# Optimization experiments

Hardware: AMD Instinct MI355X
Metric: run time of the kernel (lower is better)

The kernel has to match this reference:

```python
import jax, jax.numpy as jnp
import numpy as np
import math

D_MODEL = 1024
NUM_HEADS = 16
THETA = 10000.0


def _rope(x, pos):
    # x: [B, H, S, d_k]; pos: [S] int -- complex rotation on interleaved pairs
    d_k = x.shape[-1]
    inv_freq = 1.0 / (THETA ** (jnp.arange(0, d_k, 2, dtype=jnp.float32) / d_k))  # [d_k/2]
    angles = pos.astype(jnp.float32)[:, None] * inv_freq[None, :]  # [S, d_k/2]
    cos, sin = jnp.cos(angles), jnp.sin(angles)
    xe = x[..., 0::2]  # real parts
    xo = x[..., 1::2]  # imag parts
    out = jnp.stack([xe * cos - xo * sin, xe * sin + xo * cos], axis=-1)
    return out.reshape(x.shape)


def setup_inputs() -> dict:
    key = jax.random.key(0)
    k1, k2, k3 = jax.random.split(key, 3)
    B, S, D = 2, 2048, D_MODEL
    w_std = math.sqrt(2.0 / (D + 3 * D))
    o_std = math.sqrt(2.0 / (D + D))
    return {
        "x": jax.random.normal(k1, (B, S, D), dtype=jnp.float32),
        "token_positions": jnp.arange(S, dtype=jnp.int32),
        "w_qkv": jax.random.normal(k2, (3 * D, D), dtype=jnp.float32) * w_std,
        "w_out": jax.random.normal(k3, (D, D), dtype=jnp.float32) * o_std,
    }


def reference(x, token_positions, w_qkv, w_out):
    B, S, D = x.shape
    H = NUM_HEADS
    d_k = D // H

    qkv = jnp.einsum('bsd,ed->bse', x, w_qkv)  # [B, S, 3D]
    q, k, v = jnp.split(qkv, 3, axis=-1)

    def to_heads(t):
        return t.reshape(B, S, H, d_k).transpose(0, 2, 1, 3)  # [B, H, S, d_k]

    q, k, v = to_heads(q), to_heads(k), to_heads(v)
    q = _rope(q, token_positions)
    k = _rope(k, token_positions)

    scores = jnp.einsum('bhqd,bhkd->bhqk', q, k) / math.sqrt(d_k)
    causal = jnp.tril(jnp.ones((S, S), dtype=bool))
    scores = jnp.where(causal, scores, -jnp.inf)
    attn = jax.nn.softmax(scores, axis=-1)
    out = jnp.einsum('bhqk,bhkd->bhqd', attn, v)  # [B, H, S, d_k]
    out = out.transpose(0, 2, 1, 3).reshape(B, S, D)
    return jnp.einsum('bsd,ed->bse', out, w_out)
```

## Files before the change

### kernel.cpp

```cpp
#include <hip/hip_runtime.h>

typedef unsigned short u16;
typedef unsigned int u32;
typedef __attribute__((ext_vector_type(8))) __bf16 bf16x8;
typedef __attribute__((ext_vector_type(4))) float f32x4;
typedef __attribute__((ext_vector_type(4))) u32 u32x4;
typedef __attribute__((ext_vector_type(4))) u16 u16x4;

#define DEV __device__ __forceinline__

constexpr int S_LEN = 2048;
constexpr int DMODEL = 1024;
constexpr int NHEAD = 16;
constexpr int ROWS = 4096;
constexpr int LDP = 1056;
constexpr float QSCALE = 0.125f * 1.4426950408889634f;

DEV u16 f2bf(float f) {
  union { float f; u32 u; } v; v.f = f;
  u32 u = v.u;
  u32 r = (u + 0x7fffu + ((u >> 16) & 1u)) >> 16;
  return (u16)r;
}
DEV float vexp2(float x) {
#if __has_builtin(__builtin_amdgcn_exp2f)
  return __builtin_amdgcn_exp2f(x);
#else
  return exp2f(x);
#endif
}
DEV int swz(int r, int c) { return r * 64 + (c ^ ((r & 7) << 3)); }

__global__ __launch_bounds__(256) void k_cvt_all(const float* __restrict__ x,
                                                 const float* __restrict__ wq,
                                                 const float* __restrict__ wo,
                                                 u16* __restrict__ xb,
                                                 u16* __restrict__ wqb,
                                                 u16* __restrict__ wob) {
  int i = blockIdx.x * 256 + threadIdx.x;
  const float* in; u16* out; int off;
  if (i < 524288)       { in = x;  out = xb;  off = i; }
  else if (i < 917504)  { in = wq; out = wqb; off = i - 524288; }
  else                  { in = wo; out = wob; off = i - 917504; }
  const float4* p4 = (const float4*)in;
  float4 a = p4[2 * off], b = p4[2 * off + 1];
  alignas(16) u16 r[8] = {f2bf(a.x), f2bf(a.y), f2bf(a.z), f2bf(a.w),
                          f2bf(b.x), f2bf(b.y), f2bf(b.z), f2bf(b.w)};
  int row = off >> 7, oct = off & 127;
  *(u32x4*)(out + (size_t)row * LDP + oct * 8) = *(const u32x4*)r;
}

__global__ __launch_bounds__(256) void k_rope_tab(const int* __restrict__ pos,
                                                  float2* __restrict__ tab) {
  int t = blockIdx.x * 256 + threadIdx.x;
  int s = t >> 5, fi = t & 31;
  float p = (float)pos[s];
  float invf = expf(-(float)fi * 0.28782313662425572f);
  float ang = p * invf;
  tab[t] = float2{cosf(ang), sinf(ang)};
}

template <int BM, int MODE>
__global__ __launch_bounds__(256, 4) void k_gemm(const u16* __restrict__ A, int lda,
                                                 const u16* __restrict__ Bw, int ldb,
                                                 void* __restrict__ Out,
                                                 u16* __restrict__ vt,
                                                 const float2* __restrict__ tab,
                                                 int NB) {
  constexpr int MR = BM / 32;
  constexpr int NA = BM / 64;
  __shared__ alignas(16) u16 As[2][BM * 32];
  __shared__ alignas(16) u16 Bs[2][128 * 32];
  const int tid = threadIdx.x, lane = tid & 63;
  const int w = tid >> 6, wr = w >> 1, wc = w & 1;
  const int l15 = lane & 15, l16 = lane >> 4;
  const int cpx = gridDim.x >> 3;
  const int wg = (blockIdx.x & 7) * cpx + (blockIdx.x >> 3);
  const int mb = wg / NB, nb = wg - mb * NB;
  const int m0 = mb * BM, n0 = nb * 128;

  const int grow = tid >> 2, gc = tid & 3;
  const u16* aP = A + (size_t)(m0 + grow) * lda + gc * 8;
  const u16* bP = Bw + (size_t)(n0 + grow) * ldb + gc * 8;
  const size_t aStep = (size_t)64 * lda;
  const size_t bStep = (size_t)64 * ldb;
  const int wrI = grow * 32 + ((gc ^ (grow & 3)) << 3);

  u32x4 ra0, ra1, rb0, rb1;
#define LOADT(t) do { \
    ra0 = *(const u32x4*)(aP + (t) * 32); \
    if (NA == 2) ra1 = *(const u32x4*)(aP + aStep + (t) * 32); \
    rb0 = *(const u32x4*)(bP + (t) * 32); \
    rb1 = *(const u32x4*)(bP + bStep + (t) * 32); \
  } while (0)
#define WRITET(bufc) do { \
    *(u32x4*)&As[bufc][wrI] = ra0; \
    if (NA == 2) *(u32x4*)&As[bufc][wrI + 2048] = ra1; \
    *(u32x4*)&Bs[bufc][wrI] = rb0; \
    *(u32x4*)&Bs[bufc][wrI + 2048] = rb1; \
  } while (0)

  f32x4 acc[MR][4] = {};
  const int x3 = l15 & 3;

#define COMPUTE(bufc) do { \
    bf16x8 af[MR]; \
    _Pragma("unroll") \
    for (int m_ = 0; m_ < MR; m_++) \
      af[m_] = *(const bf16x8*)&As[bufc][(wr * (BM / 2) + m_ * 16 + l15) * 32 + \
                                         (((l16 ^ x3)) << 3)]; \
    __builtin_amdgcn_s_setprio(1); \
    _Pragma("unroll") \
    for (int n_ = 0; n_ < 4; n_++) { \
      bf16x8 bb = *(const bf16x8*)&Bs[bufc][(wc * 64 + n_ * 16 + l15) * 32 + \
                                            (((l16 ^ x3)) << 3)]; \
      _Pragma("unroll") \
      for (int m_ = 0; m_ < MR; m_++) \
        acc[m_][n_] = __builtin_amdgcn_mfma_f32_16x16x32_bf16(af[m_], bb, acc[m_][n_], 0, 0, 0); \
    } \
    __builtin_amdgcn_s_setprio(0); \
  } while (0)

#define BAR() do { \
    asm volatile("s_waitcnt lgkmcnt(0)" ::: "memory"); \
    __builtin_amdgcn_s_barrier(); \
  } while (0)

  LOADT(0);
  WRITET(0);
  LOADT(1);
  BAR();

  for (int t = 0; t < 32; ++t) {
    COMPUTE(t & 1);
    if (t + 1 < 32) WRITET((t + 1) & 1);
    if (t + 2 < 32) LOADT(t + 2);
    BAR();
  }
#undef LOADT
#undef WRITET
#undef COMPUTE
#undef BAR

  const int rb = m0 + wr * (BM / 2) + l16 * 4;
  const int cb = n0 + wc * 64 + l15;
  if (MODE == 0) {
    float* o = (float*)Out;
#pragma unroll
    for (int m = 0; m < MR; m++)
#pragma unroll
      for (int n = 0; n < 4; n++)
#pragma unroll
        for (int r = 0; r < 4; r++)
          o[(size_t)(rb + m * 16 + r) * 1024 + cb + n * 16] = acc[m][n][r];
  } else if (n0 >= 2048) {
#pragma unroll
    for (int m = 0; m < MR; m++)
#pragma unroll
      for (int n = 0; n < 4; n++) {
        int row = rb + m * 16, col = cb + n * 16;
        int bb = row >> 11, s = row & 2047, hd = col - 2048;
        u16x4 pk = {f2bf(acc[m][n][0]), f2bf(acc[m][n][1]),
                    f2bf(acc[m][n][2]), f2bf(acc[m][n][3])};
        *(u16x4*)&vt[(size_t)(bb * 1024 + hd) * S_LEN + s] = pk;
      }
  } else {
    u16* qk = (u16*)Out;
    const bool isq = (n0 < 1024);
#pragma unroll
    for (int m = 0; m < MR; m++) {
      int row0 = rb + m * 16;
      int s0 = row0 & 2047;
#pragma unroll
      for (int n = 0; n < 4; n++) {
        int col = cb + n * 16;
        int fi = (col & 63) >> 1;
        bool odd = col & 1;
        f32x4 v = acc[m][n];
        f32x4 p;
#pragma unroll
        for (int r = 0; r < 4; r++) p[r] = __shfl_xor(v[r], 1);
#pragma unroll
        for (int r = 0; r < 4; r++) {
          float2 cs = tab[(s0 + r) * 32 + fi];
          float xe = odd ? p[r] : v[r];
          float xo = odd ? v[r] : p[r];
          float o = odd ? (xe * cs.y + xo * cs.x) : (xe * cs.x - xo * cs.y);
          if (isq) o *= QSCALE;
          qk[(size_t)(row0 + r) * 2048 + col] = f2bf(o);
        }
      }
    }
  }
}

__global__ __launch_bounds__(256) void k_attn(const u16* __restrict__ qk,
                                              const u16* __restrict__ vt,
                                              u16* __restrict__ aout) {
  __shared__ alignas(16) u16 Ks[64 * 64];
  __shared__ alignas(16) u16 Vs[64 * 64];
  __shared__ alignas(16) u16 Ps[4][16 * 64];
  const int tid = threadIdx.x, lane = tid & 63, w = tid >> 6;
  const int l15 = lane & 15, l16 = lane >> 4;
  const int qt = 31 - blockIdx.y;
  const int q0 = qt * 64;
  const int bh = blockIdx.x, b = bh >> 4, h = bh & 15;
  const u16* qbase = qk + (size_t)b * S_LEN * 2048 + h * 64;
  const u16* kbase = qbase + 1024;
  const u16* vbase = vt + (size_t)bh * 64 * S_LEN;
  const int wq0 = q0 + w * 16;

  bf16x8 qa[2];
#pragma unroll
  for (int kb = 0; kb < 2; kb++)
    qa[kb] = *(const bf16x8*)&qbase[(size_t)(wq0 + l15) * 2048 + kb * 32 + l16 * 8];

  bf16x8 vone;
#pragma unroll
  for (int j = 0; j < 8; j++) vone[j] = (__bf16)1.0f;

  f32x4 osum[4] = {};
  f32x4 osl = {};

  const int nt = qt + 1;
  const int srow = tid >> 2, scg = (tid & 3) * 16;
  u32x4 kr0, kr1, vr0, vr1;
  {
    const u16* kp = kbase + (size_t)srow * 2048 + scg;
    kr0 = *(const u32x4*)kp; kr1 = *(const u32x4*)(kp + 8);
    const u16* vp = vbase + (size_t)srow * S_LEN + scg;
    vr0 = *(const u32x4*)vp; vr1 = *(const u32x4*)(vp + 8);
  }

  for (int t = 0; t < nt; t++) {
    const int kv0 = t * 64;
    __syncthreads();
    *(u32x4*)&Ks[swz(srow, scg)]     = kr0;
    *(u32x4*)&Ks[swz(srow, scg + 8)] = kr1;
    *(u32x4*)&Vs[swz(srow, scg)]     = vr0;
    *(u32x4*)&Vs[swz(srow, scg + 8)] = vr1;
    __syncthreads();
    if (t + 1 < nt) {
      const u16* kp = kbase + (size_t)(kv0 + 64 + srow) * 2048 + scg;
      kr0 = *(const u32x4*)kp; kr1 = *(const u32x4*)(kp + 8);
      const u16* vp = vbase + (size_t)srow * S_LEN + kv0 + 64 + scg;
      vr0 = *(const u32x4*)vp; vr1 = *(const u32x4*)(vp + 8);
    }

    f32x4 sc[4];
#pragma unroll
    for (int n = 0; n < 4; n++) {
      bf16x8 kf0 = *(const bf16x8*)&Ks[swz(n * 16 + l15, l16 * 8)];
      bf16x8 kf1 = *(const bf16x8*)&Ks[swz(n * 16 + l15, 32 + l16 * 8)];
      f32x4 z = {0.f, 0.f, 0.f, 0.f};
      z = __builtin_amdgcn_mfma_f32_16x16x32_bf16(qa[0], kf0, z, 0, 0, 0);
      sc[n] = __builtin_amdgcn_mfma_f32_16x16x32_bf16(qa[1], kf1, z, 0, 0, 0);
    }

    const bool diag = (t == nt - 1);
#pragma unroll
    for (int n = 0; n < 4; n++)
#pragma unroll
      for (int r = 0; r < 4; r++) {
        float s = sc[n][r];
        if (diag && (kv0 + n * 16 + l15 > wq0 + l16 * 4 + r)) s = -1e30f;
        float p = vexp2(s - 16.0f);
        Ps[w][swz(l16 * 4 + r, n * 16 + l15)] = f2bf(p);
      }

#pragma unroll
    for (int ks = 0; ks < 2; ks++) {
      bf16x8 pa = *(const bf16x8*)&Ps[w][swz(l15, ks * 32 + l16 * 8)];
      osl = __builtin_amdgcn_mfma_f32_16x16x32_bf16(pa, vone, osl, 0, 0, 0);
#pragma unroll
      for (int n = 0; n < 4; n++) {
        bf16x8 vb = *(const bf16x8*)&Vs[swz(n * 16 + l15, ks * 32 + l16 * 8)];
        osum[n] = __builtin_amdgcn_mfma_f32_16x16x32_bf16(pa, vb, osum[n], 0, 0, 0);
      }
    }
  }

  f32x4 inv;
#pragma unroll
  for (int r = 0; r < 4; r++) inv[r] = 1.0f / osl[r];
  u16* ob = aout + (size_t)(b * S_LEN) * LDP + h * 64;
#pragma unroll
  for (int n = 0; n < 4; n++)
#pragma unroll
    for (int r = 0; r < 4; r++) {
      int s = wq0 + l16 * 4 + r;
      ob[(size_t)s * LDP + n * 16 + l15] = f2bf(osum[n][r] * inv[r]);
    }
}

extern "C" void kernel_launch(void* const* d_in, const int* in_sizes, int n_in,
                              void* d_out, int out_size, void* d_ws, size_t ws_size,
                              hipStream_t stream) {
  const float* x = (const float*)d_in[0];
  const int* pos = (const int*)d_in[1];
  const float* wqkv = (const float*)d_in[2];
  const float* wout = (const float*)d_in[3];
  float* out = (float*)d_out;
  char* ws = (char*)d_ws;

  u16* qkb   = (u16*)(ws);
  u16* vtb   = (u16*)(ws + 16777216);
  u16* aoutb = (u16*)(ws + 25165824);
  u16* xb    = (u16*)(ws + 33816576);
  u16* wqb   = (u16*)(ws + 42467328);
  u16* wob   = (u16*)(ws + 48955392);
  float2* tab = (float2*)(ws + 51118080);
  (void)ws_size;

  k_cvt_all<<<4096, 256, 0, stream>>>(x, wqkv, wout, xb, wqb, wob);
  k_rope_tab<<<65536 / 256, 256, 0, stream>>>(pos, tab);

  k_gemm<128, 1><<<768, 256, 0, stream>>>(xb, LDP, wqb, LDP, qkb, vtb, tab, 24);

  dim3 ga(2 * NHEAD, S_LEN / 64);
  k_attn<<<ga, 256, 0, stream>>>(qkb, vtb, aoutb);

  k_gemm<64, 0><<<512, 256, 0, stream>>>(aoutb, LDP, wob, LDP, out, nullptr, nullptr, 8);
}
```

Baseline: 104.2 us.

## Use direct global-to-LDS loads with triple-buffered GEMM pipeline

Replaces the register-staged global load plus LDS write in the projection GEMM with global_load_lds DMA-style loads. It moves to three LDS buffers with prefetch distance two, using vmcnt waits and barriers, and changes the swizzle so it matches the fixed per-thread LDS destination. This removes register pressure and VALU/LDS write instructions from the main loop and deepens the overlap of loads with MFMA work. The cost is more LDS per block, lower occupancy (launch bounds go from 4 to 3), and an extra barrier per iteration.

Measured after the change: 107.0 us. 1.03x slower.

```diff
diff --git a/kernel.cpp b/kernel.cpp
--- a/kernel.cpp
+++ b/kernel.cpp
@@ -28,6 +28,10 @@
 #else
   return exp2f(x);
 #endif
+}
+DEV void gload_lds16(const u16* g, u16* l) {
+  __builtin_amdgcn_global_load_lds((const __attribute__((address_space(1))) void*)g,
+                                   (__attribute__((address_space(3))) void*)l, 16, 0, 0);
 }
 DEV int swz(int r, int c) { return r * 64 + (c ^ ((r & 7) << 3)); }
 
@@ -61,16 +65,16 @@
 }
 
 template <int BM, int MODE>
-__global__ __launch_bounds__(256, 4) void k_gemm(const u16* __restrict__ A, int lda,
+__global__ __launch_bounds__(256, 3) void k_gemm(const u16* __restrict__ A, int lda,
                                                  const u16* __restrict__ Bw, int ldb,
                                                  void* __restrict__ Out,
                                                  u16* __restrict__ vt,
                                                  const float2* __restrict__ tab,
                                                  int NB) {
   constexpr int MR = BM / 32;
-  constexpr int NA = BM / 64;
-  __shared__ alignas(16) u16 As[2][BM * 32];
-  __shared__ alignas(16) u16 Bs[2][128 * 32];
+  constexpr int ACH = BM / 64;
+  __shared__ alignas(16) u16 As[3][BM * 32];
+  __shared__ alignas(16) u16 Bs[3][128 * 32];
   const int tid = threadIdx.x, lane = tid & 63;
   const int w = tid >> 6, wr = w >> 1, wc = w & 1;
   const int l15 = lane & 15, l16 = lane >> 4;
@@ -79,41 +83,32 @@
   const int mb = wg / NB, nb = wg - mb * NB;
   const int m0 = mb * BM, n0 = nb * 128;
 
-  const int grow = tid >> 2, gc = tid & 3;
-  const u16* aP = A + (size_t)(m0 + grow) * lda + gc * 8;
-  const u16* bP = Bw + (size_t)(n0 + grow) * ldb + gc * 8;
-  const size_t aStep = (size_t)64 * lda;
-  const size_t bStep = (size_t)64 * ldb;
-  const int wrI = grow * 32 + ((gc ^ (grow & 3)) << 3);
-
-  u32x4 ra0, ra1, rb0, rb1;
-#define LOADT(t) do { \
-    ra0 = *(const u32x4*)(aP + (t) * 32); \
-    if (NA == 2) ra1 = *(const u32x4*)(aP + aStep + (t) * 32); \
-    rb0 = *(const u32x4*)(bP + (t) * 32); \
-    rb1 = *(const u32x4*)(bP + bStep + (t) * 32); \
+  const int srow = tid >> 2, gd = tid & 3;
+  const int scol = (gd ^ ((srow >> 1) & 3)) * 8;
+  const u16* aP = A + (size_t)(m0 + srow) * lda + scol;
+  const u16* bP = Bw + (size_t)(n0 + srow) * ldb + scol;
+  const int dI = tid * 8;
+
+#define STAGE(bufc, t) do { \
+    _Pragma("unroll") \
+    for (int c_ = 0; c_ < ACH; c_++) \
+      gload_lds16(aP + (size_t)(c_ * 64) * lda + (t) * 32, &As[bufc][dI + c_ * 2048]); \
+    gload_lds16(bP + (t) * 32, &Bs[bufc][dI]); \
+    gload_lds16(bP + (size_t)64 * ldb + (t) * 32, &Bs[bufc][dI + 2048]); \
   } while (0)
-#define WRITET(bufc) do { \
-    *(u32x4*)&As[bufc][wrI] = ra0; \
-    if (NA == 2) *(u32x4*)&As[bufc][wrI + 2048] = ra1; \
-    *(u32x4*)&Bs[bufc][wrI] = rb0; \
-    *(u32x4*)&Bs[bufc][wrI + 2048] = rb1; \
-  } while (0)
 
   f32x4 acc[MR][4] = {};
-  const int x3 = l15 & 3;
+  const int roff = (l16 ^ ((l15 >> 1) & 3)) * 8;
 
 #define COMPUTE(bufc) do { \
     bf16x8 af[MR]; \
     _Pragma("unroll") \
     for (int m_ = 0; m_ < MR; m_++) \
-      af[m_] = *(const bf16x8*)&As[bufc][(wr * (BM / 2) + m_ * 16 + l15) * 32 + \
-                                         (((l16 ^ x3)) << 3)]; \
+      af[m_] = *(const bf16x8*)&As[bufc][(wr * (BM / 2) + m_ * 16 + l15) * 32 + roff]; \
     __builtin_amdgcn_s_setprio(1); \
     _Pragma("unroll") \
     for (int n_ = 0; n_ < 4; n_++) { \
-      bf16x8 bb = *(const bf16x8*)&Bs[bufc][(wc * 64 + n_ * 16 + l15) * 32 + \
-                                            (((l16 ^ x3)) << 3)]; \
+      bf16x8 bb = *(const bf16x8*)&Bs[bufc][(wc * 64 + n_ * 16 + l15) * 32 + roff]; \
       _Pragma("unroll") \
       for (int m_ = 0; m_ < MR; m_++) \
         acc[m_][n_] = __builtin_amdgcn_mfma_f32_16x16x32_bf16(af[m_], bb, acc[m_][n_], 0, 0, 0); \
@@ -121,29 +116,31 @@
     __builtin_amdgcn_s_setprio(0); \
   } while (0)
 
-#define BAR() do { \
-    asm volatile("s_waitcnt lgkmcnt(0)" ::: "memory"); \
-    __builtin_amdgcn_s_barrier(); \
-  } while (0)
-
-  LOADT(0);
-  WRITET(0);
-  LOADT(1);
-  BAR();
-
+#define VW(n) asm volatile("s_waitcnt vmcnt(" #n ")" ::: "memory")
+
+  STAGE(0, 0);
+  STAGE(1, 1);
+
+  int cb = 0, sb = 2;
   for (int t = 0; t < 32; ++t) {
-    COMPUTE(t & 1);
-    if (t + 1 < 32) WRITET((t + 1) & 1);
-    if (t + 2 < 32) LOADT(t + 2);
-    BAR();
+    if (t + 2 < 32) STAGE(sb, t + 2);
+    if (BM == 128) {
+      if (t < 30) VW(8); else if (t == 30) VW(4); else VW(0);
+    } else {
+      if (t < 30) VW(6); else if (t == 30) VW(3); else VW(0);
+    }
+    __builtin_amdgcn_s_barrier();
+    COMPUTE(cb);
+    __builtin_amdgcn_s_barrier();
+    cb = (cb == 2) ? 0 : cb + 1;
+    sb = (sb == 2) ? 0 : sb + 1;
   }
-#undef LOADT
-#undef WRITET
+#undef STAGE
 #undef COMPUTE
-#undef BAR
+#undef VW
 
   const int rb = m0 + wr * (BM / 2) + l16 * 4;
-  const int cb = n0 + wc * 64 + l15;
+  const int cb2 = n0 + wc * 64 + l15;
   if (MODE == 0) {
     float* o = (float*)Out;
 #pragma unroll
@@ -152,13 +149,13 @@
       for (int n = 0; n < 4; n++)
 #pragma unroll
         for (int r = 0; r < 4; r++)
-          o[(size_t)(rb + m * 16 + r) * 1024 + cb + n * 16] = acc[m][n][r];
+          o[(size_t)(rb + m * 16 + r) * 1024 + cb2 + n * 16] = acc[m][n][r];
   } else if (n0 >= 2048) {
 #pragma unroll
     for (int m = 0; m < MR; m++)
 #pragma unroll
       for (int n = 0; n < 4; n++) {
-        int row = rb + m * 16, col = cb + n * 16;
+        int row = rb + m * 16, col = cb2 + n * 16;
         int bb = row >> 11, s = row & 2047, hd = col - 2048;
         u16x4 pk = {f2bf(acc[m][n][0]), f2bf(acc[m][n][1]),
                     f2bf(acc[m][n][2]), f2bf(acc[m][n][3])};
@@ -173,7 +170,7 @@
       int s0 = row0 & 2047;
 #pragma unroll
       for (int n = 0; n < 4; n++) {
-        int col = cb + n * 16;
+        int col = cb2 + n * 16;
         int fi = (col & 63) >> 1;
         bool odd = col & 1;
         f32x4 v = acc[m][n];
```
